# Kernel optimization log

Measured on AMD Instinct MI355X. Metric: run time of the kernel, lower is better.

## Reference

```python
import jax, jax.numpy as jnp
import numpy as np

D = 1024
N_HEAD = 16
EXP = 4
EPS = 1e-6


def setup_inputs() -> dict:
    key = jax.random.key(0)
    ks = jax.random.split(key, 7)
    s = 0.02
    return {
        "x": jax.random.normal(ks[0], (2, 2048, D), dtype=jnp.float32),
        "w_qkv": jax.random.normal(ks[1], (3 * D, D), dtype=jnp.float32) * s,
        "w_o": jax.random.normal(ks[2], (D, D), dtype=jnp.float32) * s,
        "w_up": jax.random.normal(ks[3], (EXP * D, D), dtype=jnp.float32) * s,
        "w_gate": jax.random.normal(ks[4], (EXP * D, D), dtype=jnp.float32) * s,
        "w_down": jax.random.normal(ks[5], (D, EXP * D), dtype=jnp.float32) * s,
        "scale1": jnp.ones((D,), dtype=jnp.float32),
        "scale2": jnp.ones((D,), dtype=jnp.float32),
    }


def rmsnorm(x, scale):
    return x / jnp.sqrt(jnp.mean(x * x, axis=-1, keepdims=True) + EPS) * scale


def attention(x, w_qkv, w_o):
    b, s, d = x.shape
    dh = d // N_HEAD
    qkv = x @ w_qkv.T  # [b,s,3d]
    q, k, v = jnp.split(qkv, 3, axis=-1)
    # [b,h,s,dh]
    q = q.reshape(b, s, N_HEAD, dh).transpose(0, 2, 1, 3)
    k = k.reshape(b, s, N_HEAD, dh).transpose(0, 2, 1, 3)
    v = v.reshape(b, s, N_HEAD, dh).transpose(0, 2, 1, 3)
    scores = jnp.einsum("bhqd,bhkd->bhqk", q, k) / jnp.sqrt(jnp.float32(dh))
    causal = jnp.tril(jnp.ones((s, s), dtype=bool))
    scores = jnp.where(causal, scores, -jnp.inf)
    attn = jax.nn.softmax(scores, axis=-1)
    out = jnp.einsum("bhqk,bhkd->bhqd", attn, v)
    out = out.transpose(0, 2, 1, 3).reshape(b, s, d)
    return out @ w_o.T


def mlp(x, w_up, w_gate, w_down):
    return (x @ w_up.T * jax.nn.silu(x @ w_gate.T)) @ w_down.T


def reference(x, w_qkv, w_o, w_up, w_gate, w_down, scale1, scale2):
    x = x + attention(rmsnorm(x, scale1), w_qkv, w_o)
    return x + mlp(rmsnorm(x, scale2), w_up, w_gate, w_down)
```

## Files before the change

### kernel.cpp

```cpp
#include <hip/hip_runtime.h>


typedef __attribute__((ext_vector_type(8))) short short8;
typedef __attribute__((ext_vector_type(4))) float floatx4;

#define EPI_NONE 0
#define EPI_RES  1
#define EPI_GATE 2
#define EPI_QKV  3

#define QSCALE 0.1803368801f

__device__ __forceinline__ float b2f(unsigned short u) {
  union { unsigned int i; float f; } c; c.i = ((unsigned int)u) << 16; return c.f;
}
__device__ __forceinline__ unsigned short f2b(float f) {
  union { float f; unsigned int u; } c; c.f = f;
  unsigned int r = 0x7fffu + ((c.u >> 16) & 1u);
  return (unsigned short)((c.u + r) >> 16);
}
__device__ __forceinline__ unsigned int f2b2(float a, float b) {
  return (unsigned int)f2b(a) | ((unsigned int)f2b(b) << 16);
}

__device__ __forceinline__ void load_lds16(const void* g, void* l) {
  __builtin_amdgcn_global_load_lds(
      (const __attribute__((address_space(1))) unsigned int*)g,
      (__attribute__((address_space(3))) unsigned int*)l, 16, 0, 0);
}

#define GBAR() __builtin_amdgcn_s_barrier()
#define WLG()  asm volatile("s_waitcnt lgkmcnt(0)" ::: "memory")
#define WVM(N) asm volatile("s_waitcnt vmcnt(" #N ")" ::: "memory")

__global__ __launch_bounds__(256)
void cvt_all_kernel(const float* __restrict__ wq, const float* __restrict__ wo,
                    const float* __restrict__ wu, const float* __restrict__ wg,
                    const float* __restrict__ wd,
                    unsigned short* __restrict__ oq, unsigned short* __restrict__ oo,
                    unsigned short* __restrict__ ou, unsigned short* __restrict__ og,
                    unsigned short* __restrict__ od) {
  int i = blockIdx.x * 256 + threadIdx.x;
  const float* src; unsigned short* dst; int k;
  if (i < 786432)        { src = wq; dst = oq; k = i; }
  else if (i < 1048576)  { src = wo; dst = oo; k = i - 786432; }
  else if (i < 2097152)  { src = wu; dst = ou; k = i - 1048576; }
  else if (i < 3145728)  { src = wg; dst = og; k = i - 2097152; }
  else                   { src = wd; dst = od; k = i - 3145728; }
  float4 v = ((const float4*)src)[k];
  ushort4 o;
  o.x = f2b(v.x); o.y = f2b(v.y); o.z = f2b(v.z); o.w = f2b(v.w);
  ((ushort4*)dst)[k] = o;
}

__global__ __launch_bounds__(256)
void rmsnorm_kernel(const float* __restrict__ x,
                    const float* __restrict__ scale,
                    unsigned short* __restrict__ y) {
  const int row = blockIdx.x;
  const int tid = threadIdx.x;
  const int base = row * 1024 + tid * 4;
  float4 v = *(const float4*)(x + base);
  float ss = v.x*v.x + v.y*v.y + v.z*v.z + v.w*v.w;
#pragma unroll
  for (int d = 32; d > 0; d >>= 1) ss += __shfl_down(ss, d);
  __shared__ float red[4];
  const int wave = tid >> 6, lane = tid & 63;
  if (lane == 0) red[wave] = ss;
  __syncthreads();
  float tot = red[0] + red[1] + red[2] + red[3];
  float rs = rsqrtf(tot * (1.0f/1024.0f) + 1e-6f);
  float4 sv = *(const float4*)(scale + tid * 4);
  ushort4 o;
  o.x = f2b(v.x * rs * sv.x);
  o.y = f2b(v.y * rs * sv.y);
  o.z = f2b(v.z * rs * sv.z);
  o.w = f2b(v.w * rs * sv.w);
  *(ushort4*)(y + base) = o;
}

__global__ __launch_bounds__(256)
void rmsnorm_res2_kernel(const float* __restrict__ x,
                         const float* __restrict__ p0,
                         const float* __restrict__ p1,
                         const float* __restrict__ scale,
                         float* __restrict__ x1,
                         unsigned short* __restrict__ y) {
  const int row = blockIdx.x;
  const int tid = threadIdx.x;
  const int base = row * 1024 + tid * 4;
  float4 a = *(const float4*)(x + base);
  float4 b = *(const float4*)(p0 + base);
  float4 c = *(const float4*)(p1 + base);
  float4 v;
  v.x = a.x + b.x + c.x; v.y = a.y + b.y + c.y;
  v.z = a.z + b.z + c.z; v.w = a.w + b.w + c.w;
  *(float4*)(x1 + base) = v;
  float ss = v.x*v.x + v.y*v.y + v.z*v.z + v.w*v.w;
#pragma unroll
  for (int d = 32; d > 0; d >>= 1) ss += __shfl_down(ss, d);
  __shared__ float red[4];
  const int wave = tid >> 6, lane = tid & 63;
  if (lane == 0) red[wave] = ss;
  __syncthreads();
  float tot = red[0] + red[1] + red[2] + red[3];
  float rs = rsqrtf(tot * (1.0f/1024.0f) + 1e-6f);
  float4 sv = *(const float4*)(scale + tid * 4);
  ushort4 o;
  o.x = f2b(v.x * rs * sv.x);
  o.y = f2b(v.y * rs * sv.y);
  o.z = f2b(v.z * rs * sv.z);
  o.w = f2b(v.w * rs * sv.w);
  *(ushort4*)(y + base) = o;
}

__global__ __launch_bounds__(256)
void reduce_out_kernel(const float* __restrict__ x1,
                       const float* __restrict__ p1,
                       float* outp) {
  int i = blockIdx.x * 256 + threadIdx.x;
  float4 a = ((const float4*)x1)[i];
  float4 b = ((const float4*)p1)[i];
  float4 c = ((float4*)outp)[i];
  float4 v;
  v.x = a.x + b.x + c.x; v.y = a.y + b.y + c.y;
  v.z = a.z + b.z + c.z; v.w = a.w + b.w + c.w;
  ((float4*)outp)[i] = v;
}

template<int EPI, typename OutT, typename ResT>
__global__ __launch_bounds__(256)
void gemm_bt(const unsigned short* __restrict__ A,
             const unsigned short* __restrict__ B,
             OutT* C, const ResT* R, unsigned short* VT,
             int M, int N, int K, int ldc) {
  __shared__ __align__(16) unsigned short As[128 * 32];
  __shared__ __align__(16) unsigned short Bs[128 * 32];
  const int tid = threadIdx.x;
  const int wave = tid >> 6;
  const int lane = tid & 63;
  const int m0 = blockIdx.y * 128;
  const int n0 = blockIdx.x * 128;
  const int wm = (wave & 1) * 64;
  const int wn = (wave >> 1) * 64;
  const int frow = lane & 15;
  const int fk = (lane >> 4) * 8;

  floatx4 acc[4][4];
#pragma unroll
  for (int i = 0; i < 4; ++i)
#pragma unroll
    for (int j = 0; j < 4; ++j) acc[i][j] = (floatx4){0.f, 0.f, 0.f, 0.f};

  const int srow = lane >> 2;
  const int scol = (lane & 3) * 8;
  const unsigned short* Ag  = A + (size_t)(m0 + wave * 16 + srow) * K + scol;
  const unsigned short* Ag2 = A + (size_t)(m0 + (wave + 4) * 16 + srow) * K + scol;
  const unsigned short* Bg  = B + (size_t)(n0 + wave * 16 + srow) * K + scol;
  const unsigned short* Bg2 = B + (size_t)(n0 + (wave + 4) * 16 + srow) * K + scol;

  for (int k0 = 0; k0 < K; k0 += 32) {
    __syncthreads();
    load_lds16(Ag + k0,  &As[wave * 512]);
    load_lds16(Ag2 + k0, &As[(wave + 4) * 512]);
    load_lds16(Bg + k0,  &Bs[wave * 512]);
    load_lds16(Bg2 + k0, &Bs[(wave + 4) * 512]);
    __syncthreads();
    short8 af[4], bf[4];
#pragma unroll
    for (int i = 0; i < 4; ++i) af[i] = *(const short8*)&As[(wm + 16*i + frow)*32 + fk];
#pragma unroll
    for (int j = 0; j < 4; ++j) bf[j] = *(const short8*)&Bs[(wn + 16*j + frow)*32 + fk];
#pragma unroll
    for (int i = 0; i < 4; ++i)
#pragma unroll
      for (int j = 0; j < 4; ++j)
        acc[i][j] = __builtin_amdgcn_mfma_f32_16x16x32_bf16(af[i], bf[j], acc[i][j], 0, 0, 0);
  }

  const int g4 = (lane >> 4) * 4;

  if constexpr (EPI == EPI_QKV) {
    if (n0 >= 2048) {
#pragma unroll
      for (int i = 0; i < 4; ++i) {
        const int row0 = m0 + wm + 16*i + g4;
        const int b = row0 >> 11, s0 = row0 & 2047;
#pragma unroll
        for (int j = 0; j < 4; ++j) {
          const int col = n0 + wn + 16*j + frow;
          const int dg = col - 2048;
          const int rowv = (b << 10) + dg;
          ushort4 ov;
          ov.x = f2b(acc[i][j][0]);
          ov.y = f2b(acc[i][j][1]);
          ov.z = f2b(acc[i][j][2]);
          ov.w = f2b(acc[i][j][3]);
          *(ushort4*)(VT + (size_t)rowv * 2048 + s0) = ov;
        }
      }
      return;
    }
  }

  const float qs = (EPI == EPI_QKV && n0 < 1024) ? QSCALE : 1.0f;
#pragma unroll
  for (int i = 0; i < 4; ++i) {
#pragma unroll
    for (int r = 0; r < 4; ++r) {
      const int row = m0 + wm + 16*i + g4 + r;
#pragma unroll
      for (int j = 0; j < 4; ++j) {
        const int col = n0 + wn + 16*j + frow;
        const size_t idx = (size_t)row * ldc + col;
        float v = acc[i][j][r];
        if constexpr (EPI == EPI_RES) {
          v += (float)R[idx];
        } else if constexpr (EPI == EPI_GATE) {
          float up = b2f((unsigned short)R[idx]);
          v = up * (v / (1.f + __expf(-v)));
        } else if constexpr (EPI == EPI_QKV) {
          v *= qs;
        }
        if constexpr (sizeof(OutT) == 4) C[idx] = v;
        else                             C[idx] = f2b(v);
      }
    }
  }
}

__global__ __launch_bounds__(256)
void gemm_bt_splitk(const unsigned short* __restrict__ A,
                    const unsigned short* __restrict__ B,
                    float* __restrict__ P0, float* __restrict__ P1,
                    int M, int N, int K, int Ks) {
  __shared__ __align__(16) unsigned short As[128 * 32];
  __shared__ __align__(16) unsigned short Bs[128 * 32];
  const int tid = threadIdx.x;
  const int wave = tid >> 6;
  const int lane = tid & 63;
  const int m0 = blockIdx.y * 128;
  const int n0 = blockIdx.x * 128;
  const int z = blockIdx.z;
  float* C = z ? P1 : P0;
  const int kbase = z * Ks;
  const int wm = (wave & 1) * 64;
  const int wn = (wave >> 1) * 64;
  const int frow = lane & 15;
  const int fk = (lane >> 4) * 8;

  floatx4 acc[4][4];
#pragma unroll
  for (int i = 0; i < 4; ++i)
#pragma unroll
    for (int j = 0; j < 4; ++j) acc[i][j] = (floatx4){0.f, 0.f, 0.f, 0.f};

  const int srow = lane >> 2;
  const int scol = (lane & 3) * 8;
  const unsigned short* Ag  = A + (size_t)(m0 + wave * 16 + srow) * K + kbase + scol;
  const unsigned short* Ag2 = A + (size_t)(m0 + (wave + 4) * 16 + srow) * K + kbase + scol;
  const unsigned short* Bg  = B + (size_t)(n0 + wave * 16 + srow) * K + kbase + scol;
  const unsigned short* Bg2 = B + (size_t)(n0 + (wave + 4) * 16 + srow) * K + kbase + scol;

  for (int k0 = 0; k0 < Ks; k0 += 32) {
    __syncthreads();
    load_lds16(Ag + k0,  &As[wave * 512]);
    load_lds16(Ag2 + k0, &As[(wave + 4) * 512]);
    load_lds16(Bg + k0,  &Bs[wave * 512]);
    load_lds16(Bg2 + k0, &Bs[(wave + 4) * 512]);
    __syncthreads();
    short8 af[4], bf[4];
#pragma unroll
    for (int i = 0; i < 4; ++i) af[i] = *(const short8*)&As[(wm + 16*i + frow)*32 + fk];
#pragma unroll
    for (int j = 0; j < 4; ++j) bf[j] = *(const short8*)&Bs[(wn + 16*j + frow)*32 + fk];
#pragma unroll
    for (int i = 0; i < 4; ++i)
#pragma unroll
      for (int j = 0; j < 4; ++j)
        acc[i][j] = __builtin_amdgcn_mfma_f32_16x16x32_bf16(af[i], bf[j], acc[i][j], 0, 0, 0);
  }

  const int g4 = (lane >> 4) * 4;
#pragma unroll
  for (int i = 0; i < 4; ++i)
#pragma unroll
    for (int r = 0; r < 4; ++r) {
      const int row = m0 + wm + 16*i + g4 + r;
#pragma unroll
      for (int j = 0; j < 4; ++j) {
        const int col = n0 + wn + 16*j + frow;
        C[(size_t)row * N + col] = acc[i][j][r];
      }
    }
}


#define A_OFF(q,h) (((q)*2+(h))*8192)
#define B_OFF(q,h) (32768 + ((q)*2+(h))*8192)

#define STAGE(LB, SRC, T) do {                                               \
    const unsigned short* _s = (SRC) + (size_t)r0 * 1024 + (T) * 64 + gs;    \
    load_lds16(_s,             &lds[(LB) + wave * 512]);                     \
    load_lds16(_s + 64 * 1024, &lds[(LB) + 4096 + wave * 512]);              \
  } while (0)

#define LDA4(dst, q, h) do {                                                 \
    const unsigned short* _b = &lds[A_OFF(q,h) + arow];                      \
    _Pragma("unroll")                                                        \
    for (int _i = 0; _i < 4; ++_i) {                                         \
      dst[_i][0] = *(const short8*)(_b + _i * 1024 + g0);                    \
      dst[_i][1] = *(const short8*)(_b + _i * 1024 + g1);                    \
    }                                                                        \
  } while (0)

#define LDB2(dst, q, h) do {                                                 \
    const unsigned short* _b = &lds[B_OFF(q,h) + brow];                      \
    _Pragma("unroll")                                                        \
    for (int _j = 0; _j < 2; ++_j) {                                         \
      dst[_j][0] = *(const short8*)(_b + _j * 1024 + g0);                    \
      dst[_j][1] = *(const short8*)(_b + _j * 1024 + g1);                    \
    }                                                                        \
  } while (0)

#define MMQ(aa, bb, IO, JO) do {                                             \
    _Pragma("unroll")                                                        \
    for (int _i = 0; _i < 4; ++_i)                                           \
      _Pragma("unroll")                                                      \
      for (int _j = 0; _j < 2; ++_j) {                                       \
        acc[(IO)+_i][(JO)+_j] = __builtin_amdgcn_mfma_f32_16x16x32_bf16(     \
            aa[_i][0], bb[_j][0], acc[(IO)+_i][(JO)+_j], 0, 0, 0);           \
        acc[(IO)+_i][(JO)+_j] = __builtin_amdgcn_mfma_f32_16x16x32_bf16(     \
            aa[_i][1], bb[_j][1], acc[(IO)+_i][(JO)+_j], 0, 0, 0);           \
      }                                                                      \
  } while (0)

__global__ __launch_bounds__(512, 2)
void gemm256_upgate(const unsigned short* __restrict__ A,
                    const unsigned short* __restrict__ Bu,
                    const unsigned short* __restrict__ Bg,
                    unsigned short* __restrict__ C) {
  extern __shared__ __align__(16) unsigned short lds[];
  const int tid  = threadIdx.x;
  const int wave = tid >> 6;
  const int lane = tid & 63;
  const int wr   = wave >> 2;
  const int wc   = wave & 3;
  const int frow = lane & 15;
  const int s4   = lane >> 4;

  const int orig = blockIdx.x;
  const int swz  = (orig & 7) * 64 + (orig >> 3);
  const int bx   = swz & 31;
  const int by   = swz >> 5;
  const int m0   = by * 256;
  const int n0   = bx * 128;

  const int f7 = frow & 7;
  const int g0 = ((0 + s4) ^ f7) * 8;
  const int g1 = ((4 + s4) ^ f7) * 8;
  const int arow = (wr * 64 + frow) * 64;
  const int brow = (wc * 32 + frow) * 64;

  const int r0 = wave * 8 + (lane >> 3);
  const int gs = ((lane & 7) ^ (lane >> 3)) * 8;

  const unsigned short* Asrc  = A  + (size_t)m0 * 1024;
  const unsigned short* B0src = Bu + (size_t)(bx * 128) * 1024;
  const unsigned short* B1src = Bg + (size_t)(bx * 128) * 1024;

  floatx4 acc[8][4];
#pragma unroll
  for (int i = 0; i < 8; ++i)
#pragma unroll
    for (int j = 0; j < 4; ++j) acc[i][j] = (floatx4){0.f, 0.f, 0.f, 0.f};

  STAGE(A_OFF(0,0), Asrc, 0);
  STAGE(B_OFF(0,0), B0src, 0);
  STAGE(B_OFF(0,1), B1src, 0);
  STAGE(A_OFF(0,1), Asrc + 128 * 1024, 0);
  WVM(4);
  STAGE(A_OFF(1,0), Asrc, 1);
  STAGE(B_OFF(1,0), B0src, 1);
  STAGE(B_OFF(1,1), B1src, 1);
  WVM(6);
  GBAR();

  short8 af0[4][2], af1[4][2], bf0[2][2], bf1[2][2];

  for (int it = 0; it < 8; ++it) {
    const int t   = it * 2;
    const int tn2 = (t + 2) & 15;
    const int tn3 = (t + 3) & 15;
    LDA4(af0, 0, 0);
    LDB2(bf0, 0, 0);
    STAGE(A_OFF(1,1), Asrc + 128 * 1024, (t + 1) & 15);
    GBAR(); WLG();
    __builtin_amdgcn_s_setprio(1); MMQ(af0, bf0, 0, 0); __builtin_amdgcn_s_setprio(0);
    GBAR();
    LDB2(bf1, 0, 1);
    STAGE(A_OFF(0,0), Asrc, tn2);
    GBAR(); WLG();
    __builtin_amdgcn_s_setprio(1); MMQ(af0, bf1, 0, 2); __builtin_amdgcn_s_setprio(0);
    GBAR();
    LDA4(af1, 0, 1);
    STAGE(B_OFF(0,0), B0src, tn2);
    GBAR(); WLG();
    __builtin_amdgcn_s_setprio(1); MMQ(af1, bf0, 4, 0); __builtin_amdgcn_s_setprio(0);
    GBAR();
    STAGE(B_OFF(0,1), B1src, tn2);
    GBAR();
    __builtin_amdgcn_s_setprio(1); MMQ(af1, bf1, 4, 2); __builtin_amdgcn_s_setprio(0);
    WVM(6);
    GBAR();
    LDA4(af0, 1, 0);
    LDB2(bf0, 1, 0);
    STAGE(A_OFF(0,1), Asrc + 128 * 1024, tn2);
    GBAR(); WLG();
    __builtin_amdgcn_s_setprio(1); MMQ(af0, bf0, 0, 0); __builtin_amdgcn_s_setprio(0);
    GBAR();
    LDB2(bf1, 1, 1);
    STAGE(A_OFF(1,0), Asrc, tn3);
    GBAR(); WLG();
    __builtin_amdgcn_s_setprio(1); MMQ(af0, bf1, 0, 2); __builtin_amdgcn_s_setprio(0);
    GBAR();
    LDA4(af1, 1, 1);
    STAGE(B_OFF(1,0), B0src, tn3);
    GBAR(); WLG();
    __builtin_amdgcn_s_setprio(1); MMQ(af1, bf0, 4, 0); __builtin_amdgcn_s_setprio(0);
    GBAR();
    STAGE(B_OFF(1,1), B1src, tn3);
    GBAR();
    __builtin_amdgcn_s_setprio(1); MMQ(af1, bf1, 4, 2); __builtin_amdgcn_s_setprio(0);
    WVM(6);
    GBAR();
  }
  asm volatile("s_waitcnt vmcnt(0)" ::: "memory");

#pragma unroll
  for (int i = 0; i < 8; ++i) {
    const int row = m0 + (i >> 2) * 128 + wr * 64 + (i & 3) * 16 + s4 * 4;
#pragma unroll
    for (int j = 0; j < 2; ++j) {
      const int col = n0 + wc * 32 + j * 16 + frow;
#pragma unroll
      for (int r = 0; r < 4; ++r) {
        const float g = acc[i][j + 2][r];
        const float v = acc[i][j][r] * (g / (1.f + __expf(-g)));
        C[(size_t)(row + r) * 4096 + col] = f2b(v);
      }
    }
  }
}

__global__ __launch_bounds__(512, 4)
void attn_kernel(const unsigned short* __restrict__ qkv,
                 const unsigned short* __restrict__ vt,
                 unsigned short* __restrict__ out) {
  __shared__ __align__(16) unsigned short Ks[2][2][128 * 32];
  __shared__ __align__(16) unsigned short Vs[2][4][64 * 32];
  const int lin = blockIdx.x;
  const int bh = lin & 31;
  const int qt = 15 - (lin >> 5);
  const int b = bh >> 4, h = bh & 15;
  const int tid = threadIdx.x, w = tid >> 6, lane = tid & 63;
  const int f = lane & 15, g = lane >> 4;
  const int fk = g * 8, g4 = g * 4;
  const int fks = (g ^ ((f >> 1) & 3)) * 8;

  const unsigned short* Qb = qkv + (size_t)(b * 2048) * 2048 + h * 64;
  const unsigned short* Kb = Qb + 1024;
  const unsigned short* Vt = vt + ((size_t)(b * 16 + h) * 64) * 2048;

  const int q0 = qt * 128 + w * 16;
  short8 qf[2];
#pragma unroll
  for (int kq = 0; kq < 2; ++kq)
    qf[kq] = *(const short8*)(Qb + (size_t)(q0 + f) * 2048 + kq * 32 + fk);

  float m_s = -1e30f, l_s = 0.f;
  floatx4 o[4];
#pragma unroll
  for (int mt = 0; mt < 4; ++mt) o[mt] = (floatx4){0.f, 0.f, 0.f, 0.f};

  const int srow = lane >> 2;
  const int scolx = ((lane & 3) ^ ((lane >> 3) & 3)) * 8;
  const int vc = w >> 1, vh = w & 1;

  auto stage = [&](int bb, int kb) {
#pragma unroll
    for (int kq = 0; kq < 2; ++kq)
      load_lds16(Kb + (size_t)(kb * 128 + w * 16 + srow) * 2048 + kq * 32 + scolx,
                 &Ks[bb][kq][w * 512]);
#pragma unroll
    for (int u = 0; u < 2; ++u)
      load_lds16(Vt + (size_t)(vh * 32 + u * 16 + srow) * 2048 + kb * 128 + vc * 32 + scolx,
                 &Vs[bb][vc][(vh * 32 + u * 16) * 32]);
  };

  stage(0, 0);

  for (int kb = 0; kb <= qt; ++kb) {
    const int cur = kb & 1;
    GBAR();
    if (kb < qt) {
      stage(cur ^ 1, kb + 1);
      WVM(4);
    } else {
      WVM(0);
    }
    GBAR();
    __builtin_amdgcn_sched_barrier(0);

    const bool diag = (kb == qt);
    const int jhi = diag ? w : 7;

    floatx4 s[8];
#pragma unroll
    for (int j = 0; j < 8; ++j) {
      if (j > jhi) continue;
      short8 kf0 = *(const short8*)&Ks[cur][0][(16*j + f) * 32 + fks];
      short8 kf1 = *(const short8*)&Ks[cur][1][(16*j + f) * 32 + fks];
      __builtin_amdgcn_s_setprio(1);
      s[j] = (floatx4){0.f, 0.f, 0.f, 0.f};
      s[j] = __builtin_amdgcn_mfma_f32_16x16x32_bf16(kf0, qf[0], s[j], 0, 0, 0);
      s[j] = __builtin_amdgcn_mfma_f32_16x16x32_bf16(kf1, qf[1], s[j], 0, 0, 0);
      __builtin_amdgcn_s_setprio(0);
    }
    if (diag) {
#pragma unroll
      for (int j = 0; j < 8; ++j) {
        if (j != w) continue;
#pragma unroll
        for (int r = 0; r < 4; ++r)
          if (g4 + r > f) s[j][r] = -1e30f;
      }
    }
    {
      float mx = -1e30f;
#pragma unroll
      for (int j = 0; j < 8; ++j) {
        if (j > jhi) continue;
#pragma unroll
        for (int r = 0; r < 4; ++r) mx = fmaxf(mx, s[j][r]);
      }
      mx = fmaxf(mx, __shfl_xor(mx, 16));
      mx = fmaxf(mx, __shfl_xor(mx, 32));
      const float mnew = fmaxf(m_s, mx);
      const float alpha = exp2f(m_s - mnew);
      float rs = 0.f;
#pragma unroll
      for (int j = 0; j < 8; ++j) {
        if (j > jhi) continue;
#pragma unroll
        for (int r = 0; r < 4; ++r) {
          float pv = exp2f(s[j][r] - mnew);
          s[j][r] = pv;
          rs += pv;
        }
      }
      rs += __shfl_xor(rs, 16);
      rs += __shfl_xor(rs, 32);
      l_s = l_s * alpha + rs;
      m_s = mnew;
#pragma unroll
      for (int mt = 0; mt < 4; ++mt) o[mt] *= alpha;
    }

    const int chi = diag ? (w >> 1) : 3;
#pragma unroll
    for (int c = 0; c < 4; ++c) {
      if (c > chi) continue;
      unsigned int P01 = f2b2(s[2*c][0], s[2*c][1]);
      unsigned int P23 = f2b2(s[2*c][2], s[2*c][3]);
      unsigned int Q01 = 0u, Q23 = 0u;
      if (2*c + 1 <= jhi) {
        Q01 = f2b2(s[2*c+1][0], s[2*c+1][1]);
        Q23 = f2b2(s[2*c+1][2], s[2*c+1][3]);
      }
      asm("v_permlane32_swap_b32 %0, %1" : "+v"(P01), "+v"(Q01));
      asm("v_permlane32_swap_b32 %0, %1" : "+v"(P23), "+v"(Q23));
      asm("v_permlane16_swap_b32 %0, %1" : "+v"(P01), "+v"(Q01));
      asm("v_permlane16_swap_b32 %0, %1" : "+v"(P23), "+v"(Q23));
      union { unsigned int d[4]; short8 v; } pbu;
      pbu.d[0] = P01; pbu.d[1] = P23; pbu.d[2] = Q01; pbu.d[3] = Q23;
#pragma unroll
      for (int mt = 0; mt < 4; ++mt) {
        short8 va = *(const short8*)&Vs[cur][c][(16*mt + f) * 32 + fks];
        __builtin_amdgcn_s_setprio(1);
        o[mt] = __builtin_amdgcn_mfma_f32_16x16x32_bf16(va, pbu.v, o[mt], 0, 0, 0);
        __builtin_amdgcn_s_setprio(0);
      }
    }
  }

  {
    const float inv = 1.0f / l_s;
    unsigned short* orow = out + (size_t)(b * 2048 + q0 + f) * 1024 + h * 64;
#pragma unroll
    for (int mt = 0; mt < 4; ++mt) {
      ushort4 ov;
      ov.x = f2b(o[mt][0] * inv);
      ov.y = f2b(o[mt][1] * inv);
      ov.z = f2b(o[mt][2] * inv);
      ov.w = f2b(o[mt][3] * inv);
      *(ushort4*)(orow + 16 * mt + g4) = ov;
    }
  }
}

extern "C" void kernel_launch(void* const* d_in, const int* in_sizes, int n_in,
                              void* d_out, int out_size, void* d_ws, size_t ws_size,
                              hipStream_t stream) {
  const float* x      = (const float*)d_in[0];
  const float* w_qkv  = (const float*)d_in[1];
  const float* w_o    = (const float*)d_in[2];
  const float* w_up   = (const float*)d_in[3];
  const float* w_gate = (const float*)d_in[4];
  const float* w_down = (const float*)d_in[5];
  const float* scale1 = (const float*)d_in[6];
  const float* scale2 = (const float*)d_in[7];

  char* ws = (char*)d_ws;
  unsigned short* wq_b = (unsigned short*)(ws);
  unsigned short* wo_b = (unsigned short*)(ws +  6291456);
  unsigned short* wu_b = (unsigned short*)(ws +  8388608);
  unsigned short* wg_b = (unsigned short*)(ws + 16777216);
  unsigned short* wd_b = (unsigned short*)(ws + 25165824);
  unsigned short* qkv  = (unsigned short*)(ws + 33554432);
  unsigned short* hup  = (unsigned short*)(ws + 33554432);
  unsigned short* vT   = (unsigned short*)(ws + 50331648);
  unsigned short* attnb= (unsigned short*)(ws + 58720256);
  unsigned short* xn   = (unsigned short*)(ws + 67108864);
  float*          x1   = (float*)         (ws + 75497472);
  float*          outp = (float*)d_out;

  float* wo_p0   = (float*)(ws + 33554432);
  float* wo_p1   = (float*)d_out;
  float* down_p0 = (float*)d_out;
  float* down_p1 = (float*)(ws + 8388608);

  const int M = 4096;
  dim3 blk(256);

  static int lds_opted = 0;
  if (!lds_opted) {
    (void)hipFuncSetAttribute((const void*)gemm256_upgate,
                              hipFuncAttributeMaxDynamicSharedMemorySize, 131072);
    lds_opted = 1;
  }

  cvt_all_kernel<<<16384, blk, 0, stream>>>(w_qkv, w_o, w_up, w_gate, w_down,
                                            wq_b, wo_b, wu_b, wg_b, wd_b);

  rmsnorm_kernel<<<4096, blk, 0, stream>>>(x, scale1, xn);
  gemm_bt<EPI_QKV, unsigned short, unsigned short>
      <<<dim3(24, 32), blk, 0, stream>>>(xn, wq_b, qkv, (const unsigned short*)nullptr, vT,
                                         M, 3072, 1024, 2048);
  attn_kernel<<<dim3(512), dim3(512), 0, stream>>>(qkv, vT, attnb);
  gemm_bt_splitk<<<dim3(8, 32, 2), blk, 0, stream>>>(attnb, wo_b, wo_p0, wo_p1,
                                                     M, 1024, 1024, 512);

  rmsnorm_res2_kernel<<<4096, blk, 0, stream>>>(x, wo_p0, wo_p1, scale2, x1, xn);

  gemm256_upgate<<<dim3(512), dim3(512), 131072, stream>>>(xn, wu_b, wg_b, hup);
  gemm_bt_splitk<<<dim3(8, 32, 2), blk, 0, stream>>>(hup, wd_b, down_p0, down_p1,
                                                     M, 1024, 4096, 2048);
  reduce_out_kernel<<<4096, blk, 0, stream>>>(x1, down_p1, outp);

  (void)in_sizes; (void)n_in; (void)out_size; (void)ws_size;
}
```

Before: 384.5 us.

## Add 256x128 pipelined split-K down-projection GEMM and XCD-aware block mapping

Replaces the generic split-K GEMM for the MLP down projection with a dedicated 256x128-tile kernel. It uses 512 threads, a multi-stage LDS pipeline, swizzled LDS staging and wave priority hints, mirroring the up/gate kernel, and writes two partial outputs over halves of K. It also changes the block-to-tile mapping of both large GEMMs so blocks on the same XCD cover neighbouring tiles, to improve L2 reuse. The new kernel needs 96 KB of dynamic LDS and only 256 blocks, which may leave some CUs underused.

```diff
diff --git a/kernel.cpp b/kernel.cpp
--- a/kernel.cpp
+++ b/kernel.cpp
@@ -295,18 +295,20 @@
     }
 }
 
-
 #define A_OFF(q,h) (((q)*2+(h))*8192)
 #define B_OFF(q,h) (32768 + ((q)*2+(h))*8192)
-
-#define STAGE(LB, SRC, T) do {                                               \
-    const unsigned short* _s = (SRC) + (size_t)r0 * 1024 + (T) * 64 + gs;    \
-    load_lds16(_s,             &lds[(LB) + wave * 512]);                     \
-    load_lds16(_s + 64 * 1024, &lds[(LB) + 4096 + wave * 512]);              \
+#define BD_OFF(q)  (32768 + (q)*8192)
+
+#define STAGE_S(LB, SRC, T, STR) do {                                        \
+    const unsigned short* _s = (SRC) + (size_t)r0 * (STR) + (T) * 64 + gs;   \
+    load_lds16(_s,                    &lds[(LB) + wave * 512]);              \
+    load_lds16(_s + (size_t)64*(STR), &lds[(LB) + 4096 + wave * 512]);       \
   } while (0)
 
-#define LDA4(dst, q, h) do {                                                 \
-    const unsigned short* _b = &lds[A_OFF(q,h) + arow];                      \
+#define STAGE(LB, SRC, T) STAGE_S(LB, SRC, T, 1024)
+
+#define LDA4X(dst, BASE) do {                                                \
+    const unsigned short* _b = &lds[(BASE) + arow];                          \
     _Pragma("unroll")                                                        \
     for (int _i = 0; _i < 4; ++_i) {                                         \
       dst[_i][0] = *(const short8*)(_b + _i * 1024 + g0);                    \
@@ -314,14 +316,17 @@
     }                                                                        \
   } while (0)
 
-#define LDB2(dst, q, h) do {                                                 \
-    const unsigned short* _b = &lds[B_OFF(q,h) + brow];                      \
+#define LDB2X(dst, BASE) do {                                                \
+    const unsigned short* _b = &lds[(BASE) + brow];                          \
     _Pragma("unroll")                                                        \
     for (int _j = 0; _j < 2; ++_j) {                                         \
       dst[_j][0] = *(const short8*)(_b + _j * 1024 + g0);                    \
       dst[_j][1] = *(const short8*)(_b + _j * 1024 + g1);                    \
     }                                                                        \
   } while (0)
+
+#define LDA4(dst, q, h) LDA4X(dst, A_OFF(q,h))
+#define LDB2(dst, q, h) LDB2X(dst, B_OFF(q,h))
 
 #define MMQ(aa, bb, IO, JO) do {                                             \
     _Pragma("unroll")                                                        \
@@ -350,9 +355,9 @@
   const int s4   = lane >> 4;
 
   const int orig = blockIdx.x;
-  const int swz  = (orig & 7) * 64 + (orig >> 3);
-  const int bx   = swz & 31;
-  const int by   = swz >> 5;
+  const int xcd  = orig & 7, l = orig >> 3;
+  const int by   = (xcd >> 2) * 8 + (l >> 3);
+  const int bx   = (xcd & 3) * 8 + (l & 7);
   const int m0   = by * 256;
   const int n0   = bx * 128;
 
@@ -449,6 +454,101 @@
         const float v = acc[i][j][r] * (g / (1.f + __expf(-g)));
         C[(size_t)(row + r) * 4096 + col] = f2b(v);
       }
+    }
+  }
+}
+
+__global__ __launch_bounds__(512, 2)
+void gemm256_down(const unsigned short* __restrict__ A,
+                  const unsigned short* __restrict__ B,
+                  float* __restrict__ P0, float* __restrict__ P1) {
+  extern __shared__ __align__(16) unsigned short lds[];
+  const int tid  = threadIdx.x;
+  const int wave = tid >> 6;
+  const int lane = tid & 63;
+  const int wr   = wave >> 2;
+  const int wc   = wave & 3;
+  const int frow = lane & 15;
+  const int s4   = lane >> 4;
+
+  const int orig = blockIdx.x;
+  const int xcd  = orig & 7, l = orig >> 3;
+  const int z    = l & 1;
+  const int by   = xcd * 2 + ((l >> 1) & 1);
+  const int bx   = l >> 2;
+  const int m0   = by * 256;
+  const int n0   = bx * 128;
+  float* P = z ? P1 : P0;
+
+  const int f7 = frow & 7;
+  const int g0 = ((0 + s4) ^ f7) * 8;
+  const int g1 = ((4 + s4) ^ f7) * 8;
+  const int arow = (wr * 64 + frow) * 64;
+  const int brow = (wc * 32 + frow) * 64;
+  const int r0 = wave * 8 + (lane >> 3);
+  const int gs = ((lane & 7) ^ (lane >> 3)) * 8;
+
+  const unsigned short* Asrc = A + (size_t)m0 * 4096 + z * 2048;
+  const unsigned short* Bsrc = B + (size_t)n0 * 4096 + z * 2048;
+
+  floatx4 acc[8][2];
+#pragma unroll
+  for (int i = 0; i < 8; ++i)
+#pragma unroll
+    for (int j = 0; j < 2; ++j) acc[i][j] = (floatx4){0.f, 0.f, 0.f, 0.f};
+
+  STAGE_S(A_OFF(0,0), Asrc, 0, 4096);
+  STAGE_S(BD_OFF(0),  Bsrc, 0, 4096);
+  STAGE_S(A_OFF(0,1), Asrc + (size_t)128 * 4096, 0, 4096);
+  STAGE_S(A_OFF(1,0), Asrc, 1, 4096);
+  STAGE_S(BD_OFF(1),  Bsrc, 1, 4096);
+  WVM(4);
+  GBAR();
+
+  short8 af0[4][2], af1[4][2], bf[2][2];
+
+  for (int it = 0; it < 16; ++it) {
+    const int t   = it * 2;
+    const int tn2 = (t + 2) & 31;
+    const int tn3 = (t + 3) & 31;
+    LDA4(af0, 0, 0);
+    LDB2X(bf, BD_OFF(0));
+    STAGE_S(A_OFF(1,1), Asrc + (size_t)128 * 4096, (t + 1) & 31, 4096);
+    GBAR(); WLG();
+    __builtin_amdgcn_s_setprio(1); MMQ(af0, bf, 0, 0); __builtin_amdgcn_s_setprio(0);
+    GBAR();
+    LDA4(af1, 0, 1);
+    STAGE_S(A_OFF(0,0), Asrc, tn2, 4096);
+    STAGE_S(BD_OFF(0),  Bsrc, tn2, 4096);
+    GBAR(); WLG();
+    __builtin_amdgcn_s_setprio(1); MMQ(af1, bf, 4, 0); __builtin_amdgcn_s_setprio(0);
+    WVM(4);
+    GBAR();
+    LDA4(af0, 1, 0);
+    LDB2X(bf, BD_OFF(1));
+    STAGE_S(A_OFF(0,1), Asrc + (size_t)128 * 4096, tn2, 4096);
+    GBAR(); WLG();
+    __builtin_amdgcn_s_setprio(1); MMQ(af0, bf, 0, 0); __builtin_amdgcn_s_setprio(0);
+    GBAR();
+    LDA4(af1, 1, 1);
+    STAGE_S(A_OFF(1,0), Asrc, tn3, 4096);
+    STAGE_S(BD_OFF(1),  Bsrc, tn3, 4096);
+    GBAR(); WLG();
+    __builtin_amdgcn_s_setprio(1); MMQ(af1, bf, 4, 0); __builtin_amdgcn_s_setprio(0);
+    WVM(4);
+    GBAR();
+  }
+  asm volatile("s_waitcnt vmcnt(0)" ::: "memory");
+
+#pragma unroll
+  for (int i = 0; i < 8; ++i) {
+    const int row = m0 + (i >> 2) * 128 + wr * 64 + (i & 3) * 16 + s4 * 4;
+#pragma unroll
+    for (int j = 0; j < 2; ++j) {
+      const int col = n0 + wc * 32 + j * 16 + frow;
+#pragma unroll
+      for (int r = 0; r < 4; ++r)
+        P[(size_t)(row + r) * 1024 + col] = acc[i][j][r];
     }
   }
 }
@@ -647,6 +747,8 @@
   if (!lds_opted) {
     (void)hipFuncSetAttribute((const void*)gemm256_upgate,
                               hipFuncAttributeMaxDynamicSharedMemorySize, 131072);
+    (void)hipFuncSetAttribute((const void*)gemm256_down,
+                              hipFuncAttributeMaxDynamicSharedMemorySize, 98304);
     lds_opted = 1;
   }
 
@@ -664,8 +766,7 @@
   rmsnorm_res2_kernel<<<4096, blk, 0, stream>>>(x, wo_p0, wo_p1, scale2, x1, xn);
 
   gemm256_upgate<<<dim3(512), dim3(512), 131072, stream>>>(xn, wu_b, wg_b, hup);
-  gemm_bt_splitk<<<dim3(8, 32, 2), blk, 0, stream>>>(hup, wd_b, down_p0, down_p1,
-                                                     M, 1024, 4096, 2048);
+  gemm256_down<<<dim3(256), dim3(512), 98304, stream>>>(hup, wd_b, down_p0, down_p1);
   reduce_out_kernel<<<4096, blk, 0, stream>>>(x1, down_p1, outp);
 
   (void)in_sizes; (void)n_in; (void)out_size; (void)ws_size;
```

Measured after the change: 357.4 us. -7.0%, faster.
